# Optimization experiments

Hardware: AMD Instinct MI355X
Metric: run time of the kernel (lower is better)

Reference implementation:

```python
import jax, jax.numpy as jnp
import numpy as np


def setup_inputs() -> dict:
    key = jax.random.key(0)
    B = 64          # number of utterances (segments)
    N = 16384       # total frames = sum(segment_num)
    D = 1024        # embedding_size
    A = 2048        # attention_dim
    H = 8           # attention_head_num
    k1, k2, k3, k4 = jax.random.split(key, 4)
    # ragged segment lengths, all >= 1, summing exactly to N
    rng = np.random.default_rng(0)
    lens = rng.integers(64, 512, size=B).astype(np.float64)
    lens = np.maximum(1, (lens * N / lens.sum()).astype(np.int64))
    lens[-1] += N - lens.sum()
    assert lens.sum() == N and (lens > 0).all()
    segment_num = jnp.asarray(lens, dtype=jnp.int32)
    x = jax.random.normal(k1, (N, D), jnp.float32)
    # torch Linear weights, stored pre-transposed as [in, out]
    w1 = jax.random.normal(k2, (D, A), jnp.float32) / np.sqrt(D)
    w2 = jax.random.normal(k3, (A, H), jnp.float32) / np.sqrt(A)
    # post_fc: Linear(D*H -> D, bias=False), stored as [D*H, D]
    w_post = jax.random.normal(k4, (D * H, D), jnp.float32) / np.sqrt(D * H)
    return {"x": x, "segment_num": segment_num, "w1": w1, "w2": w2, "w_post": w_post}


def reference(x, segment_num, w1, w2, w_post):
    N, D = x.shape
    B = segment_num.shape[0]
    H = w2.shape[1]
    # segment id for every frame (ragged -> flat segment ids)
    seg_ids = jnp.repeat(jnp.arange(B), segment_num, total_repeat_length=N)  # [N]

    # MultiAtt.w1: Linear -> ReLU -> Linear, per frame
    h = jnp.maximum(x @ w1, 0.0) @ w2  # [N, H]

    # per-segment softmax over the time axis (dim 0 within each segment)
    m = jax.ops.segment_max(h, seg_ids, num_segments=B)          # [B, H]
    p = jnp.exp(h - m[seg_ids])                                  # [N, H]
    s = jax.ops.segment_sum(p, seg_ids, num_segments=B)          # [B, H]
    attn = p / s[seg_ids]                                        # [N, H]

    # per-segment x^T @ attn -> [B, D, H] (matches torch.mm(x.T, attn))
    out_bdh = jax.ops.segment_sum(x[:, :, None] * attn[:, None, :], seg_ids, num_segments=B)
    # flatten row-major over (D, H) like out.view(-1), then post_fc (no bias)
    out = out_bdh.reshape(B, D * H) @ w_post                     # [B, D]

    # attn_i = attn^T @ attn per segment -> [B, H, H]
    attn_gram = jax.ops.segment_sum(attn[:, :, None] * attn[:, None, :], seg_ids, num_segments=B)

    # segment_type == 'average': per-segment mean of frames -> [B, D]
    out_segment = jax.ops.segment_sum(x, seg_ids, num_segments=B) / segment_num[:, None].astype(x.dtype)

    return out, out_segment, attn_gram
```

## Files before the change

### kernel.cpp

```cpp
#include <hip/hip_runtime.h>
#include <hip/hip_bf16.h>

#define NB 64
#define NN 16384
#define ND 1024
#define NA 2048
#define NH 8
#define NSLOT 16
#define KSPL 64

typedef __attribute__((ext_vector_type(4))) float f32x4;
typedef __attribute__((ext_vector_type(8))) short short8;
typedef __attribute__((ext_vector_type(8))) unsigned short ushort8;

__device__ __forceinline__ unsigned short f2bf(float f) {
    unsigned int u = __float_as_uint(f);
    u = (u + 0x7fff + ((u >> 16) & 1)) >> 16;
    return (unsigned short)u;
}

__device__ __forceinline__ float bf2f(unsigned short s) {
    return __uint_as_float((unsigned int)s << 16);
}

__device__ __forceinline__ void load_lds16(const void* g, void* l) {
    __builtin_amdgcn_global_load_lds((const __attribute__((address_space(1))) void*)g,
                                     (__attribute__((address_space(3))) void*)l, 16, 0, 0);
}

__global__ __launch_bounds__(256) void k_pre(const float* __restrict__ x,
                                             const float* __restrict__ w1,
                                             const float* __restrict__ w2,
                                             const int* __restrict__ segnum,
                                             unsigned short* __restrict__ xb,
                                             unsigned short* __restrict__ w1t,
                                             unsigned short* __restrict__ w2t_hi,
                                             unsigned short* __restrict__ w2t_lo,
                                             int* __restrict__ segoff) {
    __shared__ unsigned short t[32][33];
    const int bx = blockIdx.x;
    if (bx < 8192) {
        size_t i = ((size_t)bx * 256 + threadIdx.x) * 8;
        float4 a = *(const float4*)(x + i);
        float4 b = *(const float4*)(x + i + 4);
        ushort8 o;
        o[0] = f2bf(a.x); o[1] = f2bf(a.y); o[2] = f2bf(a.z); o[3] = f2bf(a.w);
        o[4] = f2bf(b.x); o[5] = f2bf(b.y); o[6] = f2bf(b.z); o[7] = f2bf(b.w);
        *(ushort8*)(xb + i) = o;
    } else if (bx < 10240) {
        const int idx = bx - 8192;
        const int a0 = (idx & 63) * 32, d0 = (idx >> 6) * 32;
        const int tx = threadIdx.x & 31, ty4 = (threadIdx.x >> 5) * 4;
#pragma unroll
        for (int i = 0; i < 4; i++)
            t[tx][ty4 + i] = f2bf(w1[(size_t)(d0 + ty4 + i) * NA + a0 + tx]);
        __syncthreads();
#pragma unroll
        for (int i = 0; i < 4; i++)
            w1t[(size_t)(a0 + ty4 + i) * ND + d0 + tx] = t[ty4 + i][tx];
    } else {
        for (int i = threadIdx.x; i < NA * NH; i += 256) {
            int a = i >> 3, q = i & 7;
            float w = w2[i];
            unsigned short hi = f2bf(w);
            float r = w - bf2f(hi);
            w2t_hi[(size_t)q * NA + a] = hi;
            w2t_lo[(size_t)q * NA + a] = f2bf(r);
        }
        for (int i = threadIdx.x; i < NA * NH; i += 256) {
            w2t_hi[NA * NH + i] = 0;
            w2t_lo[NA * NH + i] = 0;
        }
        if (threadIdx.x == 0) {
            int a = 0;
            segoff[0] = 0;
            for (int b = 0; b < NB; b++) { a += segnum[b]; segoff[b + 1] = a; }
        }
    }
}

__global__ __launch_bounds__(256) void k_c1(const unsigned short* __restrict__ xb,
                                            const unsigned short* __restrict__ w1t,
                                            unsigned short* __restrict__ c1) {
    __shared__ unsigned short As[128 * 64];
    __shared__ unsigned short Bs[128 * 64];

    const int tid = threadIdx.x;
    const int wave = tid >> 6, lane = tid & 63;
    const int wm = wave & 1, wn = wave >> 1;
    const int m0 = blockIdx.x * 128, n0 = blockIdx.y * 128;
    const int quad = lane >> 4, lc = lane & 15;

    f32x4 acc[4][4];
#pragma unroll
    for (int i = 0; i < 4; i++)
#pragma unroll
        for (int j = 0; j < 4; j++) acc[i][j] = (f32x4){0.f, 0.f, 0.f, 0.f};

    const int srow = lane >> 3;
    const int sg = lane & 7;

    for (int k0 = 0; k0 < ND; k0 += 64) {
        __syncthreads();
#pragma unroll
        for (int i = 0; i < 4; i++) {
            int r = wave * 32 + i * 8 + srow;
            int gc = (sg ^ (r & 7)) * 8;
            load_lds16(xb + (size_t)(m0 + r) * ND + k0 + gc, As + r * 64 + sg * 8);
            load_lds16(w1t + (size_t)(n0 + r) * ND + k0 + gc, Bs + r * 64 + sg * 8);
        }
        __syncthreads();
#pragma unroll
        for (int ksub = 0; ksub < 2; ksub++) {
            short8 af[4], bf[4];
            const int lg = ksub * 4 + quad;
#pragma unroll
            for (int t = 0; t < 4; t++) {
                int m = wm * 64 + t * 16 + lc;
                af[t] = *(const short8*)&As[m * 64 + (lg ^ (m & 7)) * 8];
                int n = wn * 64 + t * 16 + lc;
                bf[t] = *(const short8*)&Bs[n * 64 + (lg ^ (n & 7)) * 8];
            }
#pragma unroll
            for (int mi = 0; mi < 4; mi++)
#pragma unroll
                for (int ni = 0; ni < 4; ni++)
                    acc[mi][ni] = __builtin_amdgcn_mfma_f32_16x16x32_bf16(
                        af[mi], bf[ni], acc[mi][ni], 0, 0, 0);
        }
    }

#pragma unroll
    for (int mi = 0; mi < 4; mi++)
#pragma unroll
        for (int ni = 0; ni < 4; ni++) {
            const int col = n0 + wn * 64 + ni * 16 + lc;
#pragma unroll
            for (int r = 0; r < 4; r++) {
                const int row = m0 + wm * 64 + mi * 16 + quad * 4 + r;
                c1[(size_t)row * NA + col] = f2bf(fmaxf(acc[mi][ni][r], 0.f));
            }
        }
}

__global__ __launch_bounds__(256) void k_h2m(const unsigned short* __restrict__ c1,
                                             const unsigned short* __restrict__ w2t_hi,
                                             const unsigned short* __restrict__ w2t_lo,
                                             float* __restrict__ h) {
    const int wave = threadIdx.x >> 6, lane = threadIdx.x & 63;
    const int quad = lane >> 4, lc = lane & 15;
    const int row0 = (blockIdx.x * 4 + wave) * 16;

    f32x4 acc = (f32x4){0.f, 0.f, 0.f, 0.f};
    const unsigned short* ap  = c1 + (size_t)(row0 + lc) * NA + quad * 8;
    const unsigned short* bhp = w2t_hi + (size_t)lc * NA + quad * 8;
    const unsigned short* blp = w2t_lo + (size_t)lc * NA + quad * 8;

#pragma unroll 4
    for (int kc = 0; kc < NA; kc += 32) {
        short8 af = *(const short8*)(ap + kc);
        short8 bh = *(const short8*)(bhp + kc);
        short8 bl = *(const short8*)(blp + kc);
        acc = __builtin_amdgcn_mfma_f32_16x16x32_bf16(af, bh, acc, 0, 0, 0);
        acc = __builtin_amdgcn_mfma_f32_16x16x32_bf16(af, bl, acc, 0, 0, 0);
    }

    if (lc < NH) {
#pragma unroll
        for (int r = 0; r < 4; r++)
            h[(size_t)(row0 + quad * 4 + r) * NH + lc] = acc[r];
    }
}

__global__ __launch_bounds__(256) void k_attn(const float* __restrict__ h,
                                              float* __restrict__ attn,
                                              const int* __restrict__ segoff,
                                              float* __restrict__ gram) {
    const int b = blockIdx.x;
    const int s0 = segoff[b], s1 = segoff[b + 1];
    const int tid = threadIdx.x;
    __shared__ float red[4][NH];
    __shared__ float mb[NH];
    __shared__ float sinv[NH];

    float mx[NH];
#pragma unroll
    for (int q = 0; q < NH; q++) mx[q] = -1e30f;
    for (int n = s0 + tid; n < s1; n += 256) {
        const float* hr = &h[(size_t)n * NH];
#pragma unroll
        for (int q = 0; q < NH; q++) mx[q] = fmaxf(mx[q], hr[q]);
    }
#pragma unroll
    for (int q = 0; q < NH; q++)
        for (int o = 1; o < 64; o <<= 1) mx[q] = fmaxf(mx[q], __shfl_xor(mx[q], o));
    const int wv = tid >> 6;
    if ((tid & 63) == 0)
        for (int q = 0; q < NH; q++) red[wv][q] = mx[q];
    __syncthreads();
    if (tid < NH)
        mb[tid] = fmaxf(fmaxf(red[0][tid], red[1][tid]), fmaxf(red[2][tid], red[3][tid]));
    __syncthreads();

    float sm[NH];
#pragma unroll
    for (int q = 0; q < NH; q++) sm[q] = 0.f;
    for (int n = s0 + tid; n < s1; n += 256) {
        const float* hr = &h[(size_t)n * NH];
#pragma unroll
        for (int q = 0; q < NH; q++) sm[q] += expf(hr[q] - mb[q]);
    }
#pragma unroll
    for (int q = 0; q < NH; q++)
        for (int o = 1; o < 64; o <<= 1) sm[q] += __shfl_xor(sm[q], o);
    if ((tid & 63) == 0)
        for (int q = 0; q < NH; q++) red[wv][q] = sm[q];
    __syncthreads();
    if (tid < NH)
        sinv[tid] = 1.0f / (red[0][tid] + red[1][tid] + red[2][tid] + red[3][tid]);
    __syncthreads();

    float g[NH][NH];
#pragma unroll
    for (int i = 0; i < NH; i++)
#pragma unroll
        for (int j = 0; j < NH; j++) g[i][j] = 0.f;

    for (int n = s0 + tid; n < s1; n += 256) {
        const float* hr = &h[(size_t)n * NH];
        float* ar = &attn[(size_t)n * NH];
        float a[NH];
#pragma unroll
        for (int q = 0; q < NH; q++) { a[q] = expf(hr[q] - mb[q]) * sinv[q]; ar[q] = a[q]; }
#pragma unroll
        for (int i = 0; i < NH; i++)
#pragma unroll
            for (int j = 0; j < NH; j++) g[i][j] += a[i] * a[j];
    }
#pragma unroll
    for (int i = 0; i < NH; i++)
#pragma unroll
        for (int j = 0; j < NH; j++)
            for (int o = 1; o < 64; o <<= 1) g[i][j] += __shfl_xor(g[i][j], o);

    __shared__ float gred[4][64];
    if ((tid & 63) == 0) {
#pragma unroll
        for (int i = 0; i < NH; i++)
#pragma unroll
            for (int j = 0; j < NH; j++) gred[wv][i * NH + j] = g[i][j];
    }
    __syncthreads();
    if (tid < 64)
        gram[(size_t)b * 64 + tid] = gred[0][tid] + gred[1][tid] + gred[2][tid] + gred[3][tid];
}

__global__ __launch_bounds__(128) void k_bdh(const unsigned short* __restrict__ xb,
                                             const float* __restrict__ attn,
                                             const int* __restrict__ segoff,
                                             float* __restrict__ bdh_part,
                                             float* __restrict__ xsum_part) {
    const int slot = blockIdx.x;
    const int b = blockIdx.y;
    const int s0 = segoff[b], s1 = segoff[b + 1];
    const int dl = threadIdx.x;

    float acc[8][NH];
    float xs[8];
#pragma unroll
    for (int dd = 0; dd < 8; dd++) {
        xs[dd] = 0.f;
#pragma unroll
        for (int q = 0; q < NH; q++) acc[dd][q] = 0.f;
    }

    for (int n = s0 + slot; n < s1; n += NSLOT) {
        ushort8 xv = *(const ushort8*)(xb + (size_t)n * ND + dl * 8);
        const float4* ap = (const float4*)&attn[(size_t)n * NH];
        float4 a0 = ap[0], a1 = ap[1];
        float aq[NH] = {a0.x, a0.y, a0.z, a0.w, a1.x, a1.y, a1.z, a1.w};
#pragma unroll
        for (int dd = 0; dd < 8; dd++) {
            float xf = bf2f(xv[dd]);
            xs[dd] += xf;
#pragma unroll
            for (int q = 0; q < NH; q++) acc[dd][q] += xf * aq[q];
        }
    }

    float* bp = bdh_part + ((size_t)slot * NB + b) * (ND * NH) + (size_t)dl * 64;
#pragma unroll
    for (int dd = 0; dd < 8; dd++) {
        *(float4*)(bp + dd * 8)     = make_float4(acc[dd][0], acc[dd][1], acc[dd][2], acc[dd][3]);
        *(float4*)(bp + dd * 8 + 4) = make_float4(acc[dd][4], acc[dd][5], acc[dd][6], acc[dd][7]);
    }
    float* xp = xsum_part + ((size_t)slot * NB + b) * ND + (size_t)dl * 8;
    *(float4*)(xp)     = make_float4(xs[0], xs[1], xs[2], xs[3]);
    *(float4*)(xp + 4) = make_float4(xs[4], xs[5], xs[6], xs[7]);
}

__global__ __launch_bounds__(256) void k_bdh_red(const float* __restrict__ bdh_part,
                                                 const float* __restrict__ xsum_part,
                                                 const int* __restrict__ segoff,
                                                 float* __restrict__ bdh,
                                                 float* __restrict__ out_segment) {
    const int gid = blockIdx.x * 256 + threadIdx.x;
    const int b = gid >> 10, d = gid & 1023;
    float4 sa = make_float4(0.f, 0.f, 0.f, 0.f);
    float4 sb = make_float4(0.f, 0.f, 0.f, 0.f);
    float xsum = 0.f;
#pragma unroll
    for (int s = 0; s < NSLOT; s++) {
        const float* p = bdh_part + ((size_t)s * NB + b) * (ND * NH) + (size_t)d * NH;
        float4 u = ((const float4*)p)[0], v = ((const float4*)p)[1];
        sa.x += u.x; sa.y += u.y; sa.z += u.z; sa.w += u.w;
        sb.x += v.x; sb.y += v.y; sb.z += v.z; sb.w += v.w;
        xsum += xsum_part[((size_t)s * NB + b) * ND + d];
    }
    float* bp = bdh + (size_t)b * (ND * NH) + (size_t)d * NH;
    ((float4*)bp)[0] = sa;
    ((float4*)bp)[1] = sb;
    const int len = segoff[b + 1] - segoff[b];
    out_segment[(size_t)b * ND + d] = xsum / (float)len;
}

__global__ __launch_bounds__(256) void k_post(const float* __restrict__ bdh,
                                              const float* __restrict__ wp,
                                              float* __restrict__ out_part) {
    __shared__ float as[32][68];
    __shared__ float bs[32][128];
    const int tid = threadIdx.x;
    const int n0 = blockIdx.x * 128;
    const int k0 = blockIdx.y * (8192 / KSPL);
    const int tr = tid >> 4, tc = tid & 15;

    float acc[4][8];
#pragma unroll
    for (int i = 0; i < 4; i++)
#pragma unroll
        for (int j = 0; j < 8; j++) acc[i][j] = 0.f;

    for (int kc = 0; kc < 8192 / KSPL; kc += 32) {
        __syncthreads();
        {
            int r = tid >> 2;
            int c = (tid & 3) * 8;
            const float4* gp = (const float4*)(bdh + (size_t)r * (ND * NH) + k0 + kc + c);
            float4 v0 = gp[0], v1 = gp[1];
            as[c + 0][r] = v0.x; as[c + 1][r] = v0.y; as[c + 2][r] = v0.z; as[c + 3][r] = v0.w;
            as[c + 4][r] = v1.x; as[c + 5][r] = v1.y; as[c + 6][r] = v1.z; as[c + 7][r] = v1.w;
        }
        {
            int r = tid >> 3;
            int c = (tid & 7) * 16;
            const float4* gp = (const float4*)(wp + (size_t)(k0 + kc + r) * ND + n0 + c);
            float4* sp = (float4*)&bs[r][c];
            sp[0] = gp[0]; sp[1] = gp[1]; sp[2] = gp[2]; sp[3] = gp[3];
        }
        __syncthreads();
#pragma unroll
        for (int k = 0; k < 32; k++) {
            float4 a  = *(const float4*)&as[k][tr * 4];
            float4 b0 = *(const float4*)&bs[k][tc * 8];
            float4 b1 = *(const float4*)&bs[k][tc * 8 + 4];
            float av[4] = {a.x, a.y, a.z, a.w};
            float bv[8] = {b0.x, b0.y, b0.z, b0.w, b1.x, b1.y, b1.z, b1.w};
#pragma unroll
            for (int i = 0; i < 4; i++)
#pragma unroll
                for (int j = 0; j < 8; j++) acc[i][j] += av[i] * bv[j];
        }
    }

    float* op = out_part + (size_t)blockIdx.y * (NB * ND);
#pragma unroll
    for (int i = 0; i < 4; i++)
#pragma unroll
        for (int j = 0; j < 8; j++)
            op[(size_t)(tr * 4 + i) * ND + n0 + tc * 8 + j] = acc[i][j];
}

__global__ __launch_bounds__(256) void k_post_red(const float* __restrict__ out_part,
                                                  float* __restrict__ out) {
    const int i = (blockIdx.x * 256 + threadIdx.x) * 4;
    float4 s = *(const float4*)(out_part + i);
#pragma unroll
    for (int p = 1; p < KSPL; p++) {
        float4 v = *(const float4*)(out_part + (size_t)p * (NB * ND) + i);
        s.x += v.x; s.y += v.y; s.z += v.z; s.w += v.w;
    }
    *(float4*)(out + i) = s;
}

extern "C" void kernel_launch(void* const* d_in, const int* in_sizes, int n_in,
                              void* d_out, int out_size, void* d_ws, size_t ws_size,
                              hipStream_t stream) {
    (void)in_sizes; (void)n_in; (void)out_size; (void)ws_size;
    const float* x      = (const float*)d_in[0];
    const int*   segnum = (const int*)d_in[1];
    const float* w1     = (const float*)d_in[2];
    const float* w2     = (const float*)d_in[3];
    const float* wpost  = (const float*)d_in[4];

    float* out         = (float*)d_out;
    float* out_segment = out + NB * ND;
    float* gram        = out + 2 * NB * ND;

    char* ws = (char*)d_ws;
    const size_t MB = 1024 * 1024;
    int*   segoff   = (int*)ws;
    float* h        = (float*)(ws + 4 * 1024);
    float* attn     = (float*)(ws + 1 * MB);
    float* bdh      = (float*)(ws + 2 * MB);
    unsigned short* w2t_hi = (unsigned short*)(ws + 4 * MB);
    unsigned short* w2t_lo = (unsigned short*)(ws + 4 * MB + 64 * 1024);
    unsigned short* xb  = (unsigned short*)(ws + 5 * MB);
    unsigned short* w1t = (unsigned short*)(ws + 37 * MB);
    unsigned short* c1  = (unsigned short*)(ws + 41 * MB);
    float* bdh_part  = (float*)(ws + 41 * MB);
    float* xsum_part = (float*)(ws + 73 * MB);
    float* out_part  = (float*)(ws + 77 * MB);

    k_pre<<<10241, 256, 0, stream>>>(x, w1, w2, segnum, xb, w1t, w2t_hi, w2t_lo, segoff);
    k_c1<<<dim3(NN / 128, NA / 128), 256, 0, stream>>>(xb, w1t, c1);
    k_h2m<<<NN / 64, 256, 0, stream>>>(c1, w2t_hi, w2t_lo, h);
    k_attn<<<NB, 256, 0, stream>>>(h, attn, segoff, gram);
    k_bdh<<<dim3(NSLOT, NB), 128, 0, stream>>>(xb, attn, segoff, bdh_part, xsum_part);
    k_bdh_red<<<256, 256, 0, stream>>>(bdh_part, xsum_part, segoff, bdh, out_segment);
    k_post<<<dim3(ND / 128, KSPL), 256, 0, stream>>>(bdh, wpost, out_part);
    k_post_red<<<(NB * ND) / (256 * 4), 256, 0, stream>>>(out_part, out);
}
```

Baseline: 320.7 us.

## Fuse second MLP layer into first GEMM epilogue with split-K partial heads

The ReLU(x@w1) tile is now staged in LDS and multiplied by the matching w2 slice (hi/lo bf16 split) inside the first GEMM kernel. Each of the 16 column blocks writes a partial h, and the attention kernel sums these partials. This removes the 64 MB bf16 intermediate c1 and its write/read round trip, along with a separate kernel launch. In exchange it adds a 16-way partial-h buffer that the attention kernel must read, which it caches in LDS for segments up to 1024 frames. It also adds an extra LDS epilogue and more shared memory per GEMM block.

```diff
diff --git a/kernel.cpp b/kernel.cpp
--- a/kernel.cpp
+++ b/kernel.cpp
@@ -8,6 +8,7 @@
 #define NH 8
 #define NSLOT 16
 #define KSPL 64
+#define NPL 16
 
 typedef __attribute__((ext_vector_type(4))) float f32x4;
 typedef __attribute__((ext_vector_type(8))) short short8;
@@ -30,12 +31,9 @@
 
 __global__ __launch_bounds__(256) void k_pre(const float* __restrict__ x,
                                              const float* __restrict__ w1,
-                                             const float* __restrict__ w2,
                                              const int* __restrict__ segnum,
                                              unsigned short* __restrict__ xb,
                                              unsigned short* __restrict__ w1t,
-                                             unsigned short* __restrict__ w2t_hi,
-                                             unsigned short* __restrict__ w2t_lo,
                                              int* __restrict__ segoff) {
     __shared__ unsigned short t[32][33];
     const int bx = blockIdx.x;
@@ -59,18 +57,6 @@
         for (int i = 0; i < 4; i++)
             w1t[(size_t)(a0 + ty4 + i) * ND + d0 + tx] = t[ty4 + i][tx];
     } else {
-        for (int i = threadIdx.x; i < NA * NH; i += 256) {
-            int a = i >> 3, q = i & 7;
-            float w = w2[i];
-            unsigned short hi = f2bf(w);
-            float r = w - bf2f(hi);
-            w2t_hi[(size_t)q * NA + a] = hi;
-            w2t_lo[(size_t)q * NA + a] = f2bf(r);
-        }
-        for (int i = threadIdx.x; i < NA * NH; i += 256) {
-            w2t_hi[NA * NH + i] = 0;
-            w2t_lo[NA * NH + i] = 0;
-        }
         if (threadIdx.x == 0) {
             int a = 0;
             segoff[0] = 0;
@@ -79,17 +65,31 @@
     }
 }
 
-__global__ __launch_bounds__(256) void k_c1(const unsigned short* __restrict__ xb,
-                                            const unsigned short* __restrict__ w1t,
-                                            unsigned short* __restrict__ c1) {
-    __shared__ unsigned short As[128 * 64];
-    __shared__ unsigned short Bs[128 * 64];
+__global__ __launch_bounds__(256) void k_c1h(const unsigned short* __restrict__ xb,
+                                             const unsigned short* __restrict__ w1t,
+                                             const float* __restrict__ w2,
+                                             float* __restrict__ h_part) {
+    __shared__ unsigned short SM[21760];
+    unsigned short* As  = SM;
+    unsigned short* Bs  = SM + 8192;
+    unsigned short* c1s = SM;
+    unsigned short* w2hi = SM + 17408;
+    unsigned short* w2lo = SM + 19584;
 
     const int tid = threadIdx.x;
     const int wave = tid >> 6, lane = tid & 63;
     const int wm = wave & 1, wn = wave >> 1;
     const int m0 = blockIdx.x * 128, n0 = blockIdx.y * 128;
     const int quad = lane >> 4, lc = lane & 15;
+
+    for (int i = tid; i < 2176; i += 256) { w2hi[i] = 0; w2lo[i] = 0; }
+    for (int i = tid; i < 1024; i += 256) {
+        int k = i >> 3, q = i & 7;
+        float w = w2[(size_t)(n0 + k) * NH + q];
+        unsigned short hi = f2bf(w);
+        w2hi[q * 136 + k] = hi;
+        w2lo[q * 136 + k] = f2bf(w - bf2f(hi));
+    }
 
     f32x4 acc[4][4];
 #pragma unroll
@@ -130,71 +130,87 @@
         }
     }
 
+    __syncthreads();
 #pragma unroll
     for (int mi = 0; mi < 4; mi++)
 #pragma unroll
         for (int ni = 0; ni < 4; ni++) {
-            const int col = n0 + wn * 64 + ni * 16 + lc;
+            const int col = wn * 64 + ni * 16 + lc;
 #pragma unroll
             for (int r = 0; r < 4; r++) {
-                const int row = m0 + wm * 64 + mi * 16 + quad * 4 + r;
-                c1[(size_t)row * NA + col] = f2bf(fmaxf(acc[mi][ni][r], 0.f));
+                const int row = wm * 64 + mi * 16 + quad * 4 + r;
+                c1s[row * 136 + col] = f2bf(fmaxf(acc[mi][ni][r], 0.f));
             }
         }
-}
-
-__global__ __launch_bounds__(256) void k_h2m(const unsigned short* __restrict__ c1,
-                                             const unsigned short* __restrict__ w2t_hi,
-                                             const unsigned short* __restrict__ w2t_lo,
-                                             float* __restrict__ h) {
-    const int wave = threadIdx.x >> 6, lane = threadIdx.x & 63;
-    const int quad = lane >> 4, lc = lane & 15;
-    const int row0 = (blockIdx.x * 4 + wave) * 16;
-
-    f32x4 acc = (f32x4){0.f, 0.f, 0.f, 0.f};
-    const unsigned short* ap  = c1 + (size_t)(row0 + lc) * NA + quad * 8;
-    const unsigned short* bhp = w2t_hi + (size_t)lc * NA + quad * 8;
-    const unsigned short* blp = w2t_lo + (size_t)lc * NA + quad * 8;
-
-#pragma unroll 4
-    for (int kc = 0; kc < NA; kc += 32) {
-        short8 af = *(const short8*)(ap + kc);
-        short8 bh = *(const short8*)(bhp + kc);
-        short8 bl = *(const short8*)(blp + kc);
-        acc = __builtin_amdgcn_mfma_f32_16x16x32_bf16(af, bh, acc, 0, 0, 0);
-        acc = __builtin_amdgcn_mfma_f32_16x16x32_bf16(af, bl, acc, 0, 0, 0);
+    __syncthreads();
+
+    f32x4 hacc[2];
+    hacc[0] = (f32x4){0.f, 0.f, 0.f, 0.f};
+    hacc[1] = (f32x4){0.f, 0.f, 0.f, 0.f};
+#pragma unroll
+    for (int ks = 0; ks < 4; ks++) {
+        short8 bh = *(const short8*)&w2hi[lc * 136 + ks * 32 + quad * 8];
+        short8 bl = *(const short8*)&w2lo[lc * 136 + ks * 32 + quad * 8];
+#pragma unroll
+        for (int mt = 0; mt < 2; mt++) {
+            short8 af = *(const short8*)&c1s[(wave * 32 + mt * 16 + lc) * 136 + ks * 32 + quad * 8];
+            hacc[mt] = __builtin_amdgcn_mfma_f32_16x16x32_bf16(af, bh, hacc[mt], 0, 0, 0);
+            hacc[mt] = __builtin_amdgcn_mfma_f32_16x16x32_bf16(af, bl, hacc[mt], 0, 0, 0);
+        }
     }
 
     if (lc < NH) {
-#pragma unroll
-        for (int r = 0; r < 4; r++)
-            h[(size_t)(row0 + quad * 4 + r) * NH + lc] = acc[r];
-    }
-}
-
-__global__ __launch_bounds__(256) void k_attn(const float* __restrict__ h,
+        float* hp = h_part + (size_t)blockIdx.y * (NN * NH);
+#pragma unroll
+        for (int mt = 0; mt < 2; mt++)
+#pragma unroll
+            for (int r = 0; r < 4; r++)
+                hp[(size_t)(m0 + wave * 32 + mt * 16 + quad * 4 + r) * NH + lc] = hacc[mt][r];
+    }
+}
+
+__global__ __launch_bounds__(256) void k_attn(const float* __restrict__ h_part,
                                               float* __restrict__ attn,
                                               const int* __restrict__ segoff,
                                               float* __restrict__ gram) {
     const int b = blockIdx.x;
     const int s0 = segoff[b], s1 = segoff[b + 1];
+    const int len = s1 - s0;
     const int tid = threadIdx.x;
+    const int wv = tid >> 6;
+    __shared__ float hl[1024 * NH];
     __shared__ float red[4][NH];
     __shared__ float mb[NH];
     __shared__ float sinv[NH];
+    __shared__ float gred[4][64];
 
     float mx[NH];
 #pragma unroll
     for (int q = 0; q < NH; q++) mx[q] = -1e30f;
+
+    const bool cached = (len <= 1024);
+
     for (int n = s0 + tid; n < s1; n += 256) {
-        const float* hr = &h[(size_t)n * NH];
-#pragma unroll
-        for (int q = 0; q < NH; q++) mx[q] = fmaxf(mx[q], hr[q]);
+        float v[NH];
+#pragma unroll
+        for (int q = 0; q < NH; q++) v[q] = 0.f;
+#pragma unroll
+        for (int p = 0; p < NPL; p++) {
+            const float4* hp = (const float4*)(h_part + (size_t)p * (NN * NH) + (size_t)n * NH);
+            float4 u0 = hp[0], u1 = hp[1];
+            v[0] += u0.x; v[1] += u0.y; v[2] += u0.z; v[3] += u0.w;
+            v[4] += u1.x; v[5] += u1.y; v[6] += u1.z; v[7] += u1.w;
+        }
+        if (cached) {
+#pragma unroll
+            for (int q = 0; q < NH; q++) hl[(n - s0) * NH + q] = v[q];
+        }
+#pragma unroll
+        for (int q = 0; q < NH; q++) mx[q] = fmaxf(mx[q], v[q]);
     }
 #pragma unroll
     for (int q = 0; q < NH; q++)
         for (int o = 1; o < 64; o <<= 1) mx[q] = fmaxf(mx[q], __shfl_xor(mx[q], o));
-    const int wv = tid >> 6;
     if ((tid & 63) == 0)
         for (int q = 0; q < NH; q++) red[wv][q] = mx[q];
     __syncthreads();
@@ -206,9 +222,23 @@
 #pragma unroll
     for (int q = 0; q < NH; q++) sm[q] = 0.f;
     for (int n = s0 + tid; n < s1; n += 256) {
-        const float* hr = &h[(size_t)n * NH];
-#pragma unroll
-        for (int q = 0; q < NH; q++) sm[q] += expf(hr[q] - mb[q]);
+        float v[NH];
+        if (cached) {
+#pragma unroll
+            for (int q = 0; q < NH; q++) v[q] = hl[(n - s0) * NH + q];
+        } else {
+#pragma unroll
+            for (int q = 0; q < NH; q++) v[q] = 0.f;
+#pragma unroll
+            for (int p = 0; p < NPL; p++) {
+                const float4* hp = (const float4*)(h_part + (size_t)p * (NN * NH) + (size_t)n * NH);
+                float4 u0 = hp[0], u1 = hp[1];
+                v[0] += u0.x; v[1] += u0.y; v[2] += u0.z; v[3] += u0.w;
+                v[4] += u1.x; v[5] += u1.y; v[6] += u1.z; v[7] += u1.w;
+            }
+        }
+#pragma unroll
+        for (int q = 0; q < NH; q++) sm[q] += expf(v[q] - mb[q]);
     }
 #pragma unroll
     for (int q = 0; q < NH; q++)
@@ -227,11 +257,25 @@
         for (int j = 0; j < NH; j++) g[i][j] = 0.f;
 
     for (int n = s0 + tid; n < s1; n += 256) {
-        const float* hr = &h[(size_t)n * NH];
+        float v[NH];
+        if (cached) {
+#pragma unroll
+            for (int q = 0; q < NH; q++) v[q] = hl[(n - s0) * NH + q];
+        } else {
+#pragma unroll
+            for (int q = 0; q < NH; q++) v[q] = 0.f;
+#pragma unroll
+            for (int p = 0; p < NPL; p++) {
+                const float4* hp = (const float4*)(h_part + (size_t)p * (NN * NH) + (size_t)n * NH);
+                float4 u0 = hp[0], u1 = hp[1];
+                v[0] += u0.x; v[1] += u0.y; v[2] += u0.z; v[3] += u0.w;
+                v[4] += u1.x; v[5] += u1.y; v[6] += u1.z; v[7] += u1.w;
+            }
+        }
+        float a[NH];
         float* ar = &attn[(size_t)n * NH];
-        float a[NH];
-#pragma unroll
-        for (int q = 0; q < NH; q++) { a[q] = expf(hr[q] - mb[q]) * sinv[q]; ar[q] = a[q]; }
+#pragma unroll
+        for (int q = 0; q < NH; q++) { a[q] = expf(v[q] - mb[q]) * sinv[q]; ar[q] = a[q]; }
 #pragma unroll
         for (int i = 0; i < NH; i++)
 #pragma unroll
@@ -243,7 +287,6 @@
         for (int j = 0; j < NH; j++)
             for (int o = 1; o < 64; o <<= 1) g[i][j] += __shfl_xor(g[i][j], o);
 
-    __shared__ float gred[4][64];
     if ((tid & 63) == 0) {
 #pragma unroll
         for (int i = 0; i < NH; i++)
@@ -409,22 +452,18 @@
     char* ws = (char*)d_ws;
     const size_t MB = 1024 * 1024;
     int*   segoff   = (int*)ws;
-    float* h        = (float*)(ws + 4 * 1024);
     float* attn     = (float*)(ws + 1 * MB);
     float* bdh      = (float*)(ws + 2 * MB);
-    unsigned short* w2t_hi = (unsigned short*)(ws + 4 * MB);
-    unsigned short* w2t_lo = (unsigned short*)(ws + 4 * MB + 64 * 1024);
-    unsigned short* xb  = (unsigned short*)(ws + 5 * MB);
-    unsigned short* w1t = (unsigned short*)(ws + 37 * MB);
-    unsigned short* c1  = (unsigned short*)(ws + 41 * MB);
-    float* bdh_part  = (float*)(ws + 41 * MB);
-    float* xsum_part = (float*)(ws + 73 * MB);
-    float* out_part  = (float*)(ws + 77 * MB);
-
-    k_pre<<<10241, 256, 0, stream>>>(x, w1, w2, segnum, xb, w1t, w2t_hi, w2t_lo, segoff);
-    k_c1<<<dim3(NN / 128, NA / 128), 256, 0, stream>>>(xb, w1t, c1);
-    k_h2m<<<NN / 64, 256, 0, stream>>>(c1, w2t_hi, w2t_lo, h);
-    k_attn<<<NB, 256, 0, stream>>>(h, attn, segoff, gram);
+    float* h_part   = (float*)(ws + 4 * MB);
+    unsigned short* xb  = (unsigned short*)(ws + 12 * MB);
+    unsigned short* w1t = (unsigned short*)(ws + 44 * MB);
+    float* bdh_part  = (float*)(ws + 48 * MB);
+    float* xsum_part = (float*)(ws + 80 * MB);
+    float* out_part  = (float*)(ws + 84 * MB);
+
+    k_pre<<<10241, 256, 0, stream>>>(x, w1, segnum, xb, w1t, segoff);
+    k_c1h<<<dim3(NN / 128, NA / 128), 256, 0, stream>>>(xb, w1t, w2, h_part);
+    k_attn<<<NB, 256, 0, stream>>>(h_part, attn, segoff, gram);
     k_bdh<<<dim3(NSLOT, NB), 128, 0, stream>>>(xb, attn, segoff, bdh_part, xsum_part);
     k_bdh_red<<<256, 256, 0, stream>>>(bdh_part, xsum_part, segoff, bdh, out_segment);
     k_post<<<dim3(ND / 128, KSPL), 256, 0, stream>>>(bdh, wpost, out_part);
```

Measured after the change: 283.8 us. 11.5% less time.
